# Optimization experiments

Measured on AMD Instinct MI355X. Metric: run time of the kernel, lower is better.

The kernel has to match this reference:

```python
import jax, jax.numpy as jnp
import numpy as np

B, D, K, U = 4096, 1024, 5, 1024  # batch, input_dim, num_basis, units


def setup_inputs() -> dict:
    key = jax.random.key(0)
    k1, k2, k3 = jax.random.split(key, 3)
    x = jax.random.normal(k1, (B, D), dtype=jnp.float32)
    basis_weights = jax.random.normal(k2, (D, K, U), dtype=jnp.float32) * 0.02
    bias = jax.random.normal(k3, (U,), dtype=jnp.float32) * 0.02
    return {"x": x, "basis_weights": basis_weights, "bias": bias}


def reference(x, basis_weights, bias):
    # Polynomial basis expansion: x^0, x^1, ..., x^{K-1}  -> (B, D, K)
    num_basis = basis_weights.shape[1]
    powers = jnp.arange(num_basis, dtype=x.dtype)
    basis = x[..., None] ** powers  # x**0 == 1, matching tf.ones_like branch
    # Fused: einsum('bik,ikj->bij') followed by reduce_sum over i == 'bik,ikj->bj'.
    # Avoids materializing the (B, D, U) intermediate of the original.
    out = jnp.einsum("bik,ikj->bj", basis, basis_weights) + bias
    # tf.nn.gelu defaults to exact (non-approximate) GELU.
    return jax.nn.gelu(out, approximate=False)
```

## Files before the change

kernel.cpp:

```cpp
#include <hip/hip_runtime.h>
#include <hip/hip_bf16.h>
#include <math.h>


#define B_DIM 4096
#define D_DIM 1024
#define U_DIM 1024
#define KT2 4096
#define NKB 128

typedef unsigned short ushort_t;
typedef __attribute__((ext_vector_type(8))) short bf16x8;
typedef __attribute__((ext_vector_type(4))) float f32x4;

__device__ __forceinline__ ushort_t f2bf(float f) {
  union { float f; unsigned int u; } v;
  v.f = f;
  unsigned int r = v.u + 0x7FFFu + ((v.u >> 16) & 1u);
  return (ushort_t)(r >> 16);
}

__device__ __forceinline__ void load_lds16(const ushort_t* g, ushort_t* l) {
  __builtin_amdgcn_global_load_lds(
      (const __attribute__((address_space(1))) ushort_t*)g,
      (__attribute__((address_space(3))) ushort_t*)l, 16, 0, 0);
}

__device__ __forceinline__ float gelu_exact(float v) {
  return 0.5f * v * (1.0f + erff(v * 0.70710678118654752f));
}


__global__ __launch_bounds__(256) void basis_pack_kernel(
    const float* __restrict__ x, ushort_t* __restrict__ Ap) {
  const int t    = threadIdx.x;
  const int wave = t >> 6;
  const int lane = t & 63;
  const int kblk = blockIdx.x * 4 + wave;
  const int m16  = blockIdx.y;
  const int m    = lane & 15;
  const int ko   = lane >> 4;
  const int row  = m16 * 16 + m;
  const int i0   = kblk * 8 + ko * 2;

  const float xa = x[(size_t)row * D_DIM + i0];
  const float xb = x[(size_t)row * D_DIM + i0 + 1];
  const float xa2 = xa * xa, xb2 = xb * xb;
  ushort_t o[8];
  o[0] = f2bf(xa);  o[1] = f2bf(xa2); o[2] = f2bf(xa2 * xa); o[3] = f2bf(xa2 * xa2);
  o[4] = f2bf(xb);  o[5] = f2bf(xb2); o[6] = f2bf(xb2 * xb); o[7] = f2bf(xb2 * xb2);
  *(uint4*)(Ap + ((size_t)m16 * NKB + kblk) * 512 + lane * 8) = *(const uint4*)o;
}

__global__ __launch_bounds__(256) void w_pack_kernel(
    const float* __restrict__ W, ushort_t* __restrict__ Bp) {
  const int t    = threadIdx.x;
  const int wave = t >> 6;
  const int lane = t & 63;
  const int kblk = blockIdx.x * 4 + wave;
  const int n16  = blockIdx.y;
  const int jj   = lane & 15;
  const int ko   = lane >> 4;
  const int j    = n16 * 16 + jj;
  const int i0   = kblk * 8 + ko * 2;

  ushort_t o[8];
#pragma unroll
  for (int t2 = 0; t2 < 2; ++t2) {
    const int i = i0 + t2;
#pragma unroll
    for (int e = 0; e < 4; ++e) {
      const int r = i * 5 + e + 1;
      o[t2 * 4 + e] = f2bf(W[(size_t)r * U_DIM + j]);
    }
  }
  *(uint4*)(Bp + ((size_t)n16 * NKB + kblk) * 512 + lane * 8) = *(const uint4*)o;
}

__global__ __launch_bounds__(256) void fold_part_kernel(
    const float* __restrict__ W, float* __restrict__ part) {
  const int j = blockIdx.x * 256 + threadIdx.x;
  const int g = blockIdx.y;
  float s = 0.0f;
#pragma unroll 8
  for (int ii = 0; ii < 32; ++ii) {
    const int i = g * 32 + ii;
    s += W[(size_t)(i * 5) * U_DIM + j];
  }
  part[(size_t)g * U_DIM + j] = s;
}

__global__ __launch_bounds__(256) void fold_final_kernel(
    const float* __restrict__ part, const float* __restrict__ bias,
    float* __restrict__ bias2) {
  const int j = blockIdx.x * 256 + threadIdx.x;
  float s = bias[j];
#pragma unroll
  for (int g = 0; g < 32; ++g) s += part[(size_t)g * U_DIM + j];
  bias2[j] = s;
}

__global__ __launch_bounds__(256) void gemm_kernel(
    const ushort_t* __restrict__ Ap, const ushort_t* __restrict__ Bp,
    const float* __restrict__ bias2, float* __restrict__ C) {
  __shared__ ushort_t lds[2][24 * 512];

  const int tid  = threadIdx.x;
  const int wave = tid >> 6;
  const int lane = tid & 63;
  const int wm   = wave >> 1;
  const int wn   = wave & 1;
  const int m16b = blockIdx.y * 4;
  const int n16b = blockIdx.x * 8;

  const ushort_t* gsrc[6];
  int ldst[6];
#pragma unroll
  for (int s = 0; s < 6; ++s) {
    const int u  = s * 4 + wave;
    const int ku = (u >= 12) ? 1 : 0;
    const int r  = u - ku * 12;
    const ushort_t* base = (r < 4)
        ? Ap + ((size_t)(m16b + r) * NKB) * 512
        : Bp + ((size_t)(n16b + (r - 4)) * NKB) * 512;
    gsrc[s] = base + (size_t)ku * 512 + lane * 8;
    ldst[s] = u * 512 + lane * 8;
  }

  f32x4 acc[2][4];
  const f32x4 zero = {0.0f, 0.0f, 0.0f, 0.0f};
#pragma unroll
  for (int mf = 0; mf < 2; ++mf)
#pragma unroll
    for (int nf = 0; nf < 4; ++nf) acc[mf][nf] = zero;

#define STAGE(bb, it)                                                   \
  do {                                                                  \
    _Pragma("unroll")                                                   \
    for (int s = 0; s < 6; ++s)                                         \
      load_lds16(gsrc[s] + (size_t)(it) * 1024, &lds[bb][ldst[s]]);     \
  } while (0)

  STAGE(0, 0);
  __syncthreads();

  for (int it = 0; it < 64; ++it) {
    const int cur = it & 1;
    if (it + 1 < 64) STAGE(cur ^ 1, it + 1);
#pragma unroll
    for (int ku = 0; ku < 2; ++ku) {
      bf16x8 a[2], b[4];
#pragma unroll
      for (int mf = 0; mf < 2; ++mf)
        a[mf] = *(const bf16x8*)&lds[cur][(ku * 12 + wm * 2 + mf) * 512 + lane * 8];
#pragma unroll
      for (int nf = 0; nf < 4; ++nf)
        b[nf] = *(const bf16x8*)&lds[cur][(ku * 12 + 4 + wn * 4 + nf) * 512 + lane * 8];
#pragma unroll
      for (int mf = 0; mf < 2; ++mf)
#pragma unroll
        for (int nf = 0; nf < 4; ++nf)
          acc[mf][nf] = __builtin_amdgcn_mfma_f32_16x16x32_bf16(a[mf], b[nf], acc[mf][nf], 0, 0, 0);
    }
    __syncthreads();
  }
#undef STAGE

  const int crow0 = m16b * 16 + wm * 32 + (lane >> 4) * 4;
  const int ccol0 = n16b * 16 + wn * 64 + (lane & 15);
#pragma unroll
  for (int nf = 0; nf < 4; ++nf) {
    const int col = ccol0 + nf * 16;
    const float bv = bias2[col];
#pragma unroll
    for (int mf = 0; mf < 2; ++mf) {
#pragma unroll
      for (int r = 0; r < 4; ++r) {
        const int row = crow0 + mf * 16 + r;
        C[(size_t)row * U_DIM + col] = gelu_exact(acc[mf][nf][r] + bv);
      }
    }
  }
}

__global__ void fallback_kernel(const float* __restrict__ x, const float* __restrict__ W,
                                const float* __restrict__ bias, float* __restrict__ out) {
  int j  = blockIdx.x * 256 + threadIdx.x;
  int b0 = blockIdx.y * 16;
  float acc[16];
#pragma unroll
  for (int t = 0; t < 16; ++t) acc[t] = 0.0f;
  for (int i = 0; i < D_DIM; ++i) {
    const float* wr = W + (size_t)i * 5 * U_DIM + j;
    float w0 = wr[0 * U_DIM], w1 = wr[1 * U_DIM], w2 = wr[2 * U_DIM];
    float w3 = wr[3 * U_DIM], w4 = wr[4 * U_DIM];
#pragma unroll
    for (int t = 0; t < 16; ++t) {
      float xv = x[(size_t)(b0 + t) * D_DIM + i];
      float x2 = xv * xv;
      acc[t] += w0 + xv * w1 + x2 * w2 + x2 * xv * w3 + x2 * x2 * w4;
    }
  }
  float bv = bias[j];
#pragma unroll
  for (int t = 0; t < 16; ++t)
    out[(size_t)(b0 + t) * U_DIM + j] = gelu_exact(acc[t] + bv);
}

extern "C" void kernel_launch(void* const* d_in, const int* in_sizes, int n_in,
                              void* d_out, int out_size, void* d_ws, size_t ws_size,
                              hipStream_t stream) {
  const float* x    = (const float*)d_in[0];
  const float* W    = (const float*)d_in[1];
  const float* bias = (const float*)d_in[2];
  float* out = (float*)d_out;

  const size_t szA = (size_t)B_DIM * KT2 * sizeof(ushort_t);
  const size_t szB = (size_t)U_DIM * KT2 * sizeof(ushort_t);
  const size_t szP = (size_t)32 * U_DIM * sizeof(float);
  const size_t szb = (size_t)U_DIM * sizeof(float);

  if (ws_size >= szA + szB + szP + szb) {
    ushort_t* Ap   = (ushort_t*)d_ws;
    ushort_t* Bp   = (ushort_t*)((char*)d_ws + szA);
    float*    part = (float*)((char*)d_ws + szA + szB);
    float*    b2   = (float*)((char*)d_ws + szA + szB + szP);
    basis_pack_kernel<<<dim3(NKB / 4, B_DIM / 16), 256, 0, stream>>>(x, Ap);
    w_pack_kernel<<<dim3(NKB / 4, U_DIM / 16), 256, 0, stream>>>(W, Bp);
    fold_part_kernel<<<dim3(U_DIM / 256, 32), 256, 0, stream>>>(W, part);
    fold_final_kernel<<<dim3(U_DIM / 256), 256, 0, stream>>>(part, bias, b2);
    gemm_kernel<<<dim3(U_DIM / 128, B_DIM / 64), 256, 0, stream>>>(Ap, Bp, b2, out);
  } else {
    fallback_kernel<<<dim3(U_DIM / 256, B_DIM / 16), 256, 0, stream>>>(x, W, bias, out);
  }
}
```

Measured before the change: 143.0 us.

## Fuse basis expansion into GEMM and load fragments directly from global memory

New measurement: 182.9 us. +27.9%, slower.

```diff
diff --git a/kernel.cpp b/kernel.cpp
--- a/kernel.cpp
+++ b/kernel.cpp
@@ -20,37 +20,26 @@
   return (ushort_t)(r >> 16);
 }
 
-__device__ __forceinline__ void load_lds16(const ushort_t* g, ushort_t* l) {
-  __builtin_amdgcn_global_load_lds(
-      (const __attribute__((address_space(1))) ushort_t*)g,
-      (__attribute__((address_space(3))) ushort_t*)l, 16, 0, 0);
-}
-
 __device__ __forceinline__ float gelu_exact(float v) {
   return 0.5f * v * (1.0f + erff(v * 0.70710678118654752f));
 }
 
-
-__global__ __launch_bounds__(256) void basis_pack_kernel(
-    const float* __restrict__ x, ushort_t* __restrict__ Ap) {
-  const int t    = threadIdx.x;
-  const int wave = t >> 6;
-  const int lane = t & 63;
-  const int kblk = blockIdx.x * 4 + wave;
-  const int m16  = blockIdx.y;
-  const int m    = lane & 15;
-  const int ko   = lane >> 4;
-  const int row  = m16 * 16 + m;
-  const int i0   = kblk * 8 + ko * 2;
-
-  const float xa = x[(size_t)row * D_DIM + i0];
-  const float xb = x[(size_t)row * D_DIM + i0 + 1];
-  const float xa2 = xa * xa, xb2 = xb * xb;
-  ushort_t o[8];
-  o[0] = f2bf(xa);  o[1] = f2bf(xa2); o[2] = f2bf(xa2 * xa); o[3] = f2bf(xa2 * xa2);
-  o[4] = f2bf(xb);  o[5] = f2bf(xb2); o[6] = f2bf(xb2 * xb); o[7] = f2bf(xb2 * xb2);
-  *(uint4*)(Ap + ((size_t)m16 * NKB + kblk) * 512 + lane * 8) = *(const uint4*)o;
-}
+__device__ __forceinline__ bf16x8 build_afrag(float xa, float xb) {
+  const float a2 = xa * xa, b2 = xb * xb;
+  float p[8] = {xa, a2, a2 * xa, a2 * a2, xb, b2, b2 * xb, b2 * b2};
+  union { bf16x8 v; unsigned int d[4]; } r;
+#pragma unroll
+  for (int i = 0; i < 4; ++i) {
+    union { float f; unsigned int u; } lo, hi;
+    lo.f = p[2 * i];
+    hi.f = p[2 * i + 1];
+    const unsigned int ul = lo.u + 0x8000u;
+    const unsigned int uh = hi.u + 0x8000u;
+    r.d[i] = (ul >> 16) | (uh & 0xFFFF0000u);
+  }
+  return r.v;
+}
+
 
 __global__ __launch_bounds__(256) void w_pack_kernel(
     const float* __restrict__ W, ushort_t* __restrict__ Bp) {
@@ -100,32 +89,27 @@
   bias2[j] = s;
 }
 
-__global__ __launch_bounds__(256) void gemm_kernel(
-    const ushort_t* __restrict__ Ap, const ushort_t* __restrict__ Bp,
+__global__ __launch_bounds__(256, 2) void gemm_kernel(
+    const float* __restrict__ x, const ushort_t* __restrict__ Bp,
     const float* __restrict__ bias2, float* __restrict__ C) {
-  __shared__ ushort_t lds[2][24 * 512];
-
   const int tid  = threadIdx.x;
   const int wave = tid >> 6;
   const int lane = tid & 63;
   const int wm   = wave >> 1;
   const int wn   = wave & 1;
+  const int n16b = blockIdx.x * 8;
   const int m16b = blockIdx.y * 4;
-  const int n16b = blockIdx.x * 8;
-
-  const ushort_t* gsrc[6];
-  int ldst[6];
-#pragma unroll
-  for (int s = 0; s < 6; ++s) {
-    const int u  = s * 4 + wave;
-    const int ku = (u >= 12) ? 1 : 0;
-    const int r  = u - ku * 12;
-    const ushort_t* base = (r < 4)
-        ? Ap + ((size_t)(m16b + r) * NKB) * 512
-        : Bp + ((size_t)(n16b + (r - 4)) * NKB) * 512;
-    gsrc[s] = base + (size_t)ku * 512 + lane * 8;
-    ldst[s] = u * 512 + lane * 8;
-  }
+
+  const float* xptr[2];
+#pragma unroll
+  for (int mf = 0; mf < 2; ++mf)
+    xptr[mf] = x + (size_t)((m16b + wm * 2 + mf) * 16 + (lane & 15)) * D_DIM
+                 + (lane >> 4) * 2;
+
+  const ushort_t* bptr[4];
+#pragma unroll
+  for (int nf = 0; nf < 4; ++nf)
+    bptr[nf] = Bp + ((size_t)(n16b + wn * 4 + nf) * NKB) * 512 + lane * 8;
 
   f32x4 acc[2][4];
   const f32x4 zero = {0.0f, 0.0f, 0.0f, 0.0f};
@@ -134,37 +118,39 @@
 #pragma unroll
     for (int nf = 0; nf < 4; ++nf) acc[mf][nf] = zero;
 
-#define STAGE(bb, it)                                                   \
-  do {                                                                  \
-    _Pragma("unroll")                                                   \
-    for (int s = 0; s < 6; ++s)                                         \
-      load_lds16(gsrc[s] + (size_t)(it) * 1024, &lds[bb][ldst[s]]);     \
-  } while (0)
-
-  STAGE(0, 0);
-  __syncthreads();
-
-  for (int it = 0; it < 64; ++it) {
-    const int cur = it & 1;
-    if (it + 1 < 64) STAGE(cur ^ 1, it + 1);
-#pragma unroll
-    for (int ku = 0; ku < 2; ++ku) {
-      bf16x8 a[2], b[4];
+  float2 xc[2];
+  bf16x8 bc[4];
+#pragma unroll
+  for (int mf = 0; mf < 2; ++mf) xc[mf] = *(const float2*)xptr[mf];
+#pragma unroll
+  for (int nf = 0; nf < 4; ++nf) bc[nf] = *(const bf16x8*)bptr[nf];
+
+#pragma unroll 2
+  for (int kb = 0; kb < NKB; ++kb) {
+    float2 xn[2];
+    bf16x8 bn[4];
+    if (kb + 1 < NKB) {
 #pragma unroll
       for (int mf = 0; mf < 2; ++mf)
-        a[mf] = *(const bf16x8*)&lds[cur][(ku * 12 + wm * 2 + mf) * 512 + lane * 8];
+        xn[mf] = *(const float2*)(xptr[mf] + (size_t)(kb + 1) * 8);
 #pragma unroll
       for (int nf = 0; nf < 4; ++nf)
-        b[nf] = *(const bf16x8*)&lds[cur][(ku * 12 + 4 + wn * 4 + nf) * 512 + lane * 8];
-#pragma unroll
-      for (int mf = 0; mf < 2; ++mf)
-#pragma unroll
-        for (int nf = 0; nf < 4; ++nf)
-          acc[mf][nf] = __builtin_amdgcn_mfma_f32_16x16x32_bf16(a[mf], b[nf], acc[mf][nf], 0, 0, 0);
-    }
-    __syncthreads();
-  }
-#undef STAGE
+        bn[nf] = *(const bf16x8*)(bptr[nf] + (size_t)(kb + 1) * 512);
+    }
+
+    const bf16x8 a0 = build_afrag(xc[0].x, xc[0].y);
+    const bf16x8 a1 = build_afrag(xc[1].x, xc[1].y);
+#pragma unroll
+    for (int nf = 0; nf < 4; ++nf) {
+      acc[0][nf] = __builtin_amdgcn_mfma_f32_16x16x32_bf16(a0, bc[nf], acc[0][nf], 0, 0, 0);
+      acc[1][nf] = __builtin_amdgcn_mfma_f32_16x16x32_bf16(a1, bc[nf], acc[1][nf], 0, 0, 0);
+    }
+
+#pragma unroll
+    for (int mf = 0; mf < 2; ++mf) xc[mf] = xn[mf];
+#pragma unroll
+    for (int nf = 0; nf < 4; ++nf) bc[nf] = bn[nf];
+  }
 
   const int crow0 = m16b * 16 + wm * 32 + (lane >> 4) * 4;
   const int ccol0 = n16b * 16 + wn * 64 + (lane & 15);
@@ -215,21 +201,18 @@
   const float* bias = (const float*)d_in[2];
   float* out = (float*)d_out;
 
-  const size_t szA = (size_t)B_DIM * KT2 * sizeof(ushort_t);
   const size_t szB = (size_t)U_DIM * KT2 * sizeof(ushort_t);
   const size_t szP = (size_t)32 * U_DIM * sizeof(float);
   const size_t szb = (size_t)U_DIM * sizeof(float);
 
-  if (ws_size >= szA + szB + szP + szb) {
-    ushort_t* Ap   = (ushort_t*)d_ws;
-    ushort_t* Bp   = (ushort_t*)((char*)d_ws + szA);
-    float*    part = (float*)((char*)d_ws + szA + szB);
-    float*    b2   = (float*)((char*)d_ws + szA + szB + szP);
-    basis_pack_kernel<<<dim3(NKB / 4, B_DIM / 16), 256, 0, stream>>>(x, Ap);
+  if (ws_size >= szB + szP + szb) {
+    ushort_t* Bp   = (ushort_t*)d_ws;
+    float*    part = (float*)((char*)d_ws + szB);
+    float*    b2   = (float*)((char*)d_ws + szB + szP);
     w_pack_kernel<<<dim3(NKB / 4, U_DIM / 16), 256, 0, stream>>>(W, Bp);
     fold_part_kernel<<<dim3(U_DIM / 256, 32), 256, 0, stream>>>(W, part);
     fold_final_kernel<<<dim3(U_DIM / 256), 256, 0, stream>>>(part, bias, b2);
-    gemm_kernel<<<dim3(U_DIM / 128, B_DIM / 64), 256, 0, stream>>>(Ap, Bp, b2, out);
+    gemm_kernel<<<dim3(U_DIM / 128, B_DIM / 64), 256, 0, stream>>>(x, Bp, b2, out);
   } else {
     fallback_kernel<<<dim3(U_DIM / 256, B_DIM / 16), 256, 0, stream>>>(x, W, bias, out);
   }
```

## Fuse weight packing with bias fold and coalesce basis packing loads

Applied to the files above, without the earlier changes.

After: 150.4 us. 5.2% more time.

```diff
diff --git a/kernel.cpp b/kernel.cpp
--- a/kernel.cpp
+++ b/kernel.cpp
@@ -33,76 +33,103 @@
 
 __global__ __launch_bounds__(256) void basis_pack_kernel(
     const float* __restrict__ x, ushort_t* __restrict__ Ap) {
-  const int t    = threadIdx.x;
-  const int wave = t >> 6;
-  const int lane = t & 63;
-  const int kblk = blockIdx.x * 4 + wave;
-  const int m16  = blockIdx.y;
-  const int m    = lane & 15;
-  const int ko   = lane >> 4;
-  const int row  = m16 * 16 + m;
-  const int i0   = kblk * 8 + ko * 2;
-
-  const float xa = x[(size_t)row * D_DIM + i0];
-  const float xb = x[(size_t)row * D_DIM + i0 + 1];
-  const float xa2 = xa * xa, xb2 = xb * xb;
-  ushort_t o[8];
-  o[0] = f2bf(xa);  o[1] = f2bf(xa2); o[2] = f2bf(xa2 * xa); o[3] = f2bf(xa2 * xa2);
-  o[4] = f2bf(xb);  o[5] = f2bf(xb2); o[6] = f2bf(xb2 * xb); o[7] = f2bf(xb2 * xb2);
-  *(uint4*)(Ap + ((size_t)m16 * NKB + kblk) * 512 + lane * 8) = *(const uint4*)o;
-}
-
-__global__ __launch_bounds__(256) void w_pack_kernel(
-    const float* __restrict__ W, ushort_t* __restrict__ Bp) {
-  const int t    = threadIdx.x;
-  const int wave = t >> 6;
-  const int lane = t & 63;
-  const int kblk = blockIdx.x * 4 + wave;
-  const int n16  = blockIdx.y;
+  const int tid = threadIdx.x;
+  const int m   = tid & 15;
+  const int q   = tid >> 4;
+  const int m16 = blockIdx.y;
+  const int row = m16 * 16 + m;
+  const float* xrow = x + (size_t)row * D_DIM;
+
+#pragma unroll
+  for (int it = 0; it < 4; ++it) {
+    const int it_g = blockIdx.x * 4 + it;
+    const int i0   = it_g * 64 + q * 4;
+    const float4 f = *(const float4*)(xrow + i0);
+
+    const int kb    = i0 >> 3;
+    const int octA  = (q & 1) * 2;
+    ushort_t oA[8], oB[8];
+    {
+      const float a = f.x, b = f.y;
+      const float a2 = a * a, b2 = b * b;
+      oA[0] = f2bf(a);  oA[1] = f2bf(a2); oA[2] = f2bf(a2 * a); oA[3] = f2bf(a2 * a2);
+      oA[4] = f2bf(b);  oA[5] = f2bf(b2); oA[6] = f2bf(b2 * b); oA[7] = f2bf(b2 * b2);
+    }
+    {
+      const float a = f.z, b = f.w;
+      const float a2 = a * a, b2 = b * b;
+      oB[0] = f2bf(a);  oB[1] = f2bf(a2); oB[2] = f2bf(a2 * a); oB[3] = f2bf(a2 * a2);
+      oB[4] = f2bf(b);  oB[5] = f2bf(b2); oB[6] = f2bf(b2 * b); oB[7] = f2bf(b2 * b2);
+    }
+    ushort_t* ub = Ap + ((size_t)m16 * NKB + kb) * 512;
+    *(uint4*)(ub + (octA * 16 + m) * 8)       = *(const uint4*)oA;
+    *(uint4*)(ub + ((octA + 1) * 16 + m) * 8) = *(const uint4*)oB;
+  }
+}
+
+__global__ __launch_bounds__(256) void w_pack_fold_kernel(
+    const float* __restrict__ W, ushort_t* __restrict__ Bp, float* __restrict__ part) {
+  __shared__ ushort_t st[256 * 34];
+  __shared__ float red[8][32];
+
+  const int tid = threadIdx.x;
+  const int bj  = blockIdx.x;
+  const int bi  = blockIdx.y;
+  const int j0  = bj * 32;
+  const int col = tid & 31;
+  const int rr  = tid >> 5;
+  const float* wbase = W + (size_t)(bi * 64) * 5 * U_DIM + j0;
+
+  float facc = 0.0f;
+#pragma unroll 8
+  for (int t = 0; t < 40; ++t) {
+    const int r_loc = t * 8 + rr;
+    const float v = wbase[(size_t)r_loc * U_DIM + col];
+    const int i_loc = r_loc / 5;
+    const int e     = r_loc - i_loc * 5;
+    if (e == 0) {
+      facc += v;
+    } else {
+      st[(i_loc * 4 + e - 1) * 34 + col] = f2bf(v);
+    }
+  }
+  red[rr][col] = facc;
+  __syncthreads();
+
+  if (tid < 32) {
+    float s = 0.0f;
+#pragma unroll
+    for (int g = 0; g < 8; ++g) s += red[g][tid];
+    part[(size_t)bi * U_DIM + j0 + tid] = s;
+  }
+
+  const int wave = tid >> 6;
+  const int lane = tid & 63;
   const int jj   = lane & 15;
   const int ko   = lane >> 4;
-  const int j    = n16 * 16 + jj;
-  const int i0   = kblk * 8 + ko * 2;
-
-  ushort_t o[8];
-#pragma unroll
-  for (int t2 = 0; t2 < 2; ++t2) {
-    const int i = i0 + t2;
-#pragma unroll
-    for (int e = 0; e < 4; ++e) {
-      const int r = i * 5 + e + 1;
-      o[t2 * 4 + e] = f2bf(W[(size_t)r * U_DIM + j]);
-    }
-  }
-  *(uint4*)(Bp + ((size_t)n16 * NKB + kblk) * 512 + lane * 8) = *(const uint4*)o;
-}
-
-__global__ __launch_bounds__(256) void fold_part_kernel(
-    const float* __restrict__ W, float* __restrict__ part) {
-  const int j = blockIdx.x * 256 + threadIdx.x;
-  const int g = blockIdx.y;
-  float s = 0.0f;
-#pragma unroll 8
-  for (int ii = 0; ii < 32; ++ii) {
-    const int i = g * 32 + ii;
-    s += W[(size_t)(i * 5) * U_DIM + j];
-  }
-  part[(size_t)g * U_DIM + j] = s;
-}
-
-__global__ __launch_bounds__(256) void fold_final_kernel(
-    const float* __restrict__ part, const float* __restrict__ bias,
-    float* __restrict__ bias2) {
-  const int j = blockIdx.x * 256 + threadIdx.x;
-  float s = bias[j];
-#pragma unroll
-  for (int g = 0; g < 32; ++g) s += part[(size_t)g * U_DIM + j];
-  bias2[j] = s;
+#pragma unroll
+  for (int s = 0; s < 4; ++s) {
+    const int u      = wave * 4 + s;
+    const int n16loc = u & 1;
+    const int kbloc  = u >> 1;
+    const int j_loc  = n16loc * 16 + jj;
+    const int i_loc0 = kbloc * 8 + ko * 2;
+    ushort_t o[8];
+#pragma unroll
+    for (int t2 = 0; t2 < 2; ++t2)
+#pragma unroll
+      for (int e = 0; e < 4; ++e)
+        o[t2 * 4 + e] = st[((i_loc0 + t2) * 4 + e) * 34 + j_loc];
+    const int n16 = bj * 2 + n16loc;
+    const int kb  = bi * 8 + kbloc;
+    *(uint4*)(Bp + ((size_t)n16 * NKB + kb) * 512 + lane * 8) = *(const uint4*)o;
+  }
 }
 
 __global__ __launch_bounds__(256) void gemm_kernel(
     const ushort_t* __restrict__ Ap, const ushort_t* __restrict__ Bp,
-    const float* __restrict__ bias2, float* __restrict__ C) {
+    const float* __restrict__ bias, const float* __restrict__ part,
+    float* __restrict__ C) {
   __shared__ ushort_t lds[2][24 * 512];
 
   const int tid  = threadIdx.x;
@@ -147,6 +174,7 @@
   for (int it = 0; it < 64; ++it) {
     const int cur = it & 1;
     if (it + 1 < 64) STAGE(cur ^ 1, it + 1);
+
 #pragma unroll
     for (int ku = 0; ku < 2; ++ku) {
       bf16x8 a[2], b[4];
@@ -171,7 +199,9 @@
 #pragma unroll
   for (int nf = 0; nf < 4; ++nf) {
     const int col = ccol0 + nf * 16;
-    const float bv = bias2[col];
+    float bv = bias[col];
+#pragma unroll
+    for (int g = 0; g < 16; ++g) bv += part[(size_t)g * U_DIM + col];
 #pragma unroll
     for (int mf = 0; mf < 2; ++mf) {
 #pragma unroll
@@ -217,19 +247,15 @@
 
   const size_t szA = (size_t)B_DIM * KT2 * sizeof(ushort_t);
   const size_t szB = (size_t)U_DIM * KT2 * sizeof(ushort_t);
-  const size_t szP = (size_t)32 * U_DIM * sizeof(float);
-  const size_t szb = (size_t)U_DIM * sizeof(float);
-
-  if (ws_size >= szA + szB + szP + szb) {
+  const size_t szP = (size_t)16 * U_DIM * sizeof(float);
+
+  if (ws_size >= szA + szB + szP) {
     ushort_t* Ap   = (ushort_t*)d_ws;
     ushort_t* Bp   = (ushort_t*)((char*)d_ws + szA);
     float*    part = (float*)((char*)d_ws + szA + szB);
-    float*    b2   = (float*)((char*)d_ws + szA + szB + szP);
-    basis_pack_kernel<<<dim3(NKB / 4, B_DIM / 16), 256, 0, stream>>>(x, Ap);
-    w_pack_kernel<<<dim3(NKB / 4, U_DIM / 16), 256, 0, stream>>>(W, Bp);
-    fold_part_kernel<<<dim3(U_DIM / 256, 32), 256, 0, stream>>>(W, part);
-    fold_final_kernel<<<dim3(U_DIM / 256), 256, 0, stream>>>(part, bias, b2);
-    gemm_kernel<<<dim3(U_DIM / 128, B_DIM / 64), 256, 0, stream>>>(Ap, Bp, b2, out);
+    basis_pack_kernel<<<dim3(4, B_DIM / 16), 256, 0, stream>>>(x, Ap);
+    w_pack_fold_kernel<<<dim3(32, 16), 256, 0, stream>>>(W, Bp, part);
+    gemm_kernel<<<dim3(U_DIM / 128, B_DIM / 64), 256, 0, stream>>>(Ap, Bp, bias, part, out);
   } else {
     fallback_kernel<<<dim3(U_DIM / 256, B_DIM / 16), 256, 0, stream>>>(x, W, bias, out);
   }
```
